# Kernel tuning notes

Hardware: AMD Instinct MI355X
Metric: run time of the kernel (lower is better)

The kernel has to match this reference:

```python
import jax, jax.numpy as jnp
import numpy as np

B, T, H = 2, 2048, 1024
DFF = 4 * H        # dense_mlp hidden width
E = 8              # num_experts_temp
TOP_K = 2


def setup_inputs() -> dict:
    key = jax.random.key(0)
    ks = jax.random.split(key, 6)
    s_h = 1.0 / np.sqrt(H)
    s_f = 1.0 / np.sqrt(DFF)
    return {
        "hidden_states": jax.random.normal(ks[0], (B, T, H), dtype=jnp.float32),
        "router_w": jax.random.normal(ks[1], (E, H), dtype=jnp.float32) * s_h,
        "w1": jax.random.normal(ks[2], (E, H, DFF), dtype=jnp.float32) * s_h,
        "b1": jnp.zeros((E, DFF), dtype=jnp.float32),
        "w2": jax.random.normal(ks[3], (E, DFF, H), dtype=jnp.float32) * s_f,
        "b2": jnp.zeros((E, H), dtype=jnp.float32),
    }


def reference(hidden_states, router_w, w1, b1, w2, b2):
    # Router: [B,T,E]
    router_logits = jnp.einsum("bth,eh->bte", hidden_states, router_w)
    topk_vals, topk_idx = jax.lax.top_k(router_logits, TOP_K)        # [B,T,K]
    topk_w = jax.nn.softmax(topk_vals.astype(jnp.float32), axis=-1)
    topk_w = topk_w.astype(hidden_states.dtype)

    # Dense compute of ALL experts (faithful to the original module).
    h = jnp.einsum("bth,ehf->btef", hidden_states, w1) + b1          # [B,T,E,DFF]
    h = jax.nn.gelu(h)
    expert_out = jnp.einsum("btef,efh->bteh", h, w2) + b2            # [B,T,E,H]

    # Gather top-k experts per token and mix.
    topk_out = jnp.take_along_axis(expert_out, topk_idx[..., None], axis=2)  # [B,T,K,H]
    mixed = jnp.sum(topk_out * topk_w[..., None], axis=2)            # [B,T,H]
    return mixed
```

## Files before the change

kernel.cpp:

```cpp
#include <hip/hip_runtime.h>
#include <hip/hip_bf16.h>
#include <stdint.h>

#define AS1 __attribute__((address_space(1)))
#define AS3 __attribute__((address_space(3)))

typedef __bf16 bf16x8 __attribute__((ext_vector_type(8)));
typedef float floatx4 __attribute__((ext_vector_type(4)));

static constexpr int NTOK = 4096;
static constexpr int H    = 1024;
static constexpr int DFF  = 4096;
static constexpr int E    = 8;
static constexpr int BN   = 128;
static constexpr int RBMAX = 72;

static constexpr size_t OFF_WS     = 0;
static constexpr size_t OFF_XCS    = 67108864;
static constexpr size_t OFF_HS     = 85983232;
static constexpr size_t OFF_P1     = 161480704;
static constexpr size_t OFF_RTIDX  = 180355072;
static constexpr size_t OFF_RTW    = 180387840;
static constexpr size_t OFF_PTOK   = 180420608;
static constexpr size_t OFF_PW     = 180457472;
static constexpr size_t OFF_TOKPOS = 180494336;
static constexpr size_t OFF_CNT    = 180527104;
static constexpr size_t WS_NEED    = 180527232;

__device__ __forceinline__ unsigned short f2bf(float f) {
    __bf16 b = (__bf16)f;
    return __builtin_bit_cast(unsigned short, b);
}
__device__ __forceinline__ float bf2f(unsigned short u) {
    unsigned int v = ((unsigned int)u) << 16;
    return __builtin_bit_cast(float, v);
}

__device__ __forceinline__ void gload16(const void* g, void* l) {
    __builtin_amdgcn_global_load_lds((AS1 void*)g, (AS3 void*)l, 16, 0, 0);
}

__global__ __launch_bounds__(256) void k_router(const float* __restrict__ x,
                                                const float* __restrict__ rw,
                                                int* __restrict__ rt_idx,
                                                float* __restrict__ rt_w,
                                                int* __restrict__ counts) {
    const int wv = threadIdx.x >> 6, ln = threadIdx.x & 63;
    const int t = blockIdx.x * 4 + wv;
    const float* xr = x + (size_t)t * H + ln * 4;
    float4 xv[4];
#pragma unroll
    for (int c = 0; c < 4; ++c) xv[c] = *(const float4*)(xr + c * 256);
    float lg[E];
#pragma unroll
    for (int e = 0; e < E; ++e) {
        const float* rr = rw + (size_t)e * H + ln * 4;
        float acc = 0.f;
#pragma unroll
        for (int c = 0; c < 4; ++c) {
            float4 rv = *(const float4*)(rr + c * 256);
            acc += xv[c].x * rv.x + xv[c].y * rv.y + xv[c].z * rv.z + xv[c].w * rv.w;
        }
#pragma unroll
        for (int s = 32; s > 0; s >>= 1) acc += __shfl_xor(acc, s, 64);
        lg[e] = acc;
    }
    if (ln == 0) {
        int i0 = 0; float v0 = lg[0];
#pragma unroll
        for (int e = 1; e < E; ++e) if (lg[e] > v0) { v0 = lg[e]; i0 = e; }
        int i1 = -1; float v1 = -INFINITY;
#pragma unroll
        for (int e = 0; e < E; ++e) if (e != i0 && lg[e] > v1) { v1 = lg[e]; i1 = e; }
        float e1 = expf(v1 - v0);
        float inv = 1.f / (1.f + e1);
        rt_idx[2 * t] = i0; rt_idx[2 * t + 1] = i1;
        rt_w[2 * t] = inv;  rt_w[2 * t + 1] = e1 * inv;
        atomicAdd(&counts[i0], 1);
        atomicAdd(&counts[i1], 1);
    }
}

__global__ void k_offsets(const int* __restrict__ counts, int* __restrict__ offs) {
    if (threadIdx.x == 0) {
        int o = 0;
        for (int e = 0; e < E; ++e) { offs[e] = o; o += (counts[e] + 127) & ~127; }
        offs[E] = o;
    }
}

__global__ __launch_bounds__(256) void k_scatter(const int* __restrict__ rt_idx,
                                                 const float* __restrict__ rt_w,
                                                 const int* __restrict__ offs,
                                                 int* __restrict__ cursors,
                                                 int* __restrict__ pair_tok,
                                                 float* __restrict__ pair_w,
                                                 int* __restrict__ tok_pos) {
    int t = blockIdx.x * 256 + threadIdx.x;
    if (t >= NTOK) return;
    for (int k = 0; k < 2; ++k) {
        int e = rt_idx[2 * t + k];
        int p = atomicAdd(&cursors[e], 1);
        int pos = offs[e] + p;
        pair_tok[pos] = t;
        pair_w[pos] = rt_w[2 * t + k];
        tok_pos[2 * t + k] = pos;
    }
}

__global__ __launch_bounds__(256) void k_gather(const float* __restrict__ x,
                                                const int* __restrict__ offs,
                                                const int* __restrict__ counts,
                                                const int* __restrict__ pair_tok,
                                                unsigned short* __restrict__ xcs) {
    int pos = blockIdx.x;
    if (pos >= offs[E]) return;
    int e = 0;
    while (e < E - 1 && pos >= offs[e + 1]) ++e;
    bool valid = (pos - offs[e]) < counts[e];
    int tok = valid ? pair_tok[pos] : 0;
    int k0 = threadIdx.x * 4;
    float4 xv = valid ? *(const float4*)(x + (size_t)tok * H + k0)
                      : make_float4(0.f, 0.f, 0.f, 0.f);
    ushort4 o;
    o.x = f2bf(xv.x); o.y = f2bf(xv.y); o.z = f2bf(xv.z); o.w = f2bf(xv.w);
    int rb = pos >> 7, m = pos & 127;
    size_t idx = (((size_t)(rb * 32 + (k0 >> 5)) * 128 + m) * 32) + (((k0 >> 3) & 3) << 3) + (k0 & 7);
    *(ushort4*)(xcs + idx) = o;
}

template <int K, int N>
__global__ __launch_bounds__(256) void k_convert(const float* __restrict__ w,
                                                 unsigned short* __restrict__ ws) {
    constexpr int KB = K / 32, NC = N / 128;
    const int bid = blockIdx.x;
    const int nc = bid % NC, kb = (bid / NC) % KB, e = bid / (NC * KB);
    const int n0 = nc * 128;
    __shared__ float lp[32][128];
    const int tid = threadIdx.x;
    {
        const int kr = tid >> 5;
        const int c4 = (tid & 31) * 4;
        const float* src = w + (size_t)(e * K + kb * 32 + kr) * N + n0 + c4;
#pragma unroll
        for (int c = 0; c < 4; ++c)
            *(float4*)&lp[kr + 8 * c][c4] = *(const float4*)(src + (size_t)(8 * c) * N);
    }
    __syncthreads();
    const size_t base = ((size_t)(e * KB + kb) * N + n0) * 4;
#pragma unroll
    for (int it = 0; it < 2; ++it) {
        const int item = it * 256 + tid;
        const int nl = item >> 2, kq = item & 3;
        union { unsigned short us[8]; uint4 v; } u;
#pragma unroll
        for (int j = 0; j < 8; ++j) u.us[j] = f2bf(lp[kq * 8 + j][nl]);
        *(uint4*)(ws + (base + (size_t)nl * 4 + kq) * 8) = u.v;
    }
}

__global__ __launch_bounds__(256) void k_gemm1(const unsigned short* __restrict__ Xc,
                                               const unsigned short* __restrict__ W1s,
                                               const int* __restrict__ offs,
                                               const float* __restrict__ b1,
                                               unsigned short* __restrict__ Hs) {
    constexpr int KB = H / 32;
    constexpr int MP = 36;
    constexpr int NB = DFF / BN;
    constexpr int CPX = NB * (RBMAX - 1) / 8;
    const int bid = blockIdx.x;
    const int t = (bid & 7) * CPX + (bid >> 3);
    const int rb = t / NB;
    if (rb * 128 >= offs[E]) return;
    int e = 0;
    while (e < E - 1 && rb * 128 >= offs[e + 1]) ++e;
    const int n0 = (t % NB) * BN;

    __shared__ unsigned short smem[4 * 128 * MP];
    unsigned short* lds_a = smem;
    unsigned short* lds_b = smem + 4096;

    const int tid = threadIdx.x;
    const int wv = tid >> 6, ln = tid & 63;
    const int quad = ln >> 4, lr = ln & 15;
    const int wm = (wv & 1) * 64, wn = (wv >> 1) * 64;

    floatx4 acc[4][4];
#pragma unroll
    for (int i = 0; i < 4; ++i)
#pragma unroll
        for (int j = 0; j < 4; ++j) acc[i][j] = (floatx4){0.f, 0.f, 0.f, 0.f};

    const unsigned short* Atile = Xc + (size_t)rb * KB * 4096;
    const unsigned short* Btile = W1s + ((size_t)e * KB * DFF + n0) * 32;

    for (int kb = 0; kb < KB; ++kb) {
        __syncthreads();
        const unsigned short* a_src = Atile + (size_t)kb * 4096 + (wv * 2) * 512 + ln * 8;
        const unsigned short* b_src = Btile + (size_t)kb * DFF * 32 + (wv * 2) * 512 + ln * 8;
#pragma unroll
        for (int c = 0; c < 2; ++c) {
            gload16(a_src + c * 512, &lds_a[(wv * 2 + c) * 512]);
            gload16(b_src + c * 512, &lds_b[(wv * 2 + c) * 512]);
        }
        __syncthreads();
        bf16x8 af[4], bg[4];
#pragma unroll
        for (int i = 0; i < 4; ++i) {
            af[i] = *(const bf16x8*)(lds_a + (wm + i * 16 + lr) * 32 + quad * 8);
            bg[i] = *(const bf16x8*)(lds_b + (wn + i * 16 + lr) * 32 + quad * 8);
        }
#pragma unroll
        for (int i = 0; i < 4; ++i)
#pragma unroll
            for (int j = 0; j < 4; ++j)
                acc[i][j] = __builtin_amdgcn_mfma_f32_16x16x32_bf16(af[i], bg[j], acc[i][j], 0, 0, 0);
    }

    float bj[4];
#pragma unroll
    for (int j = 0; j < 4; ++j) bj[j] = b1[(size_t)e * DFF + n0 + wn + j * 16 + lr];
    __syncthreads();
#pragma unroll
    for (int j = 0; j < 4; ++j) {
        const int fl = wn + j * 16 + lr;
        const int fb = fl >> 5, f5 = fl & 31;
        unsigned short* dst = smem + fb * (128 * MP) + f5;
#pragma unroll
        for (int i = 0; i < 4; ++i) {
#pragma unroll
            for (int r = 0; r < 4; ++r) {
                const int m = wm + i * 16 + quad * 4 + r;
                float v = acc[i][j][r] + bj[j];
                float u = 0.79788456080286535588f * (v + 0.044715f * v * v * v);
                float ez = __expf(2.f * u);
                float g = v * (1.f - 1.f / (ez + 1.f));
                dst[m * MP] = f2bf(g);
            }
        }
    }
    __syncthreads();
    const size_t hsbase = ((size_t)rb * 128 + (n0 >> 5)) * 4096;
#pragma unroll
    for (int it = 0; it < 8; ++it) {
        const int g = (it * 256 + tid) * 8;
        const int fb = g >> 12, rem = g & 4095, m = rem >> 5, f5 = rem & 31;
        const unsigned short* s = smem + fb * (128 * MP) + m * MP + f5;
        uint2 lo = *(const uint2*)s;
        uint2 hi = *(const uint2*)(s + 4);
        *(uint4*)(Hs + hsbase + (size_t)g) = make_uint4(lo.x, lo.y, hi.x, hi.y);
    }
}

__global__ __launch_bounds__(256) void k_gemm2(const unsigned short* __restrict__ Hs,
                                               const unsigned short* __restrict__ W2s,
                                               const int* __restrict__ offs,
                                               const float* __restrict__ b2,
                                               unsigned short* __restrict__ P0,
                                               unsigned short* __restrict__ P1) {
    constexpr int KB = DFF / 32;
    constexpr int KBS = KB / 2;
    constexpr int NB = H / BN;
    constexpr int CPX = NB * (RBMAX - 1) * 2 / 8;
    const int bid = blockIdx.x;
    const int t = (bid & 7) * CPX + (bid >> 3);
    const int yz = t >> 3;
    const int rb = yz % (RBMAX - 1);
    const int ks = yz / (RBMAX - 1);
    if (rb * 128 >= offs[E]) return;
    int e = 0;
    while (e < E - 1 && rb * 128 >= offs[e + 1]) ++e;
    const int n0 = (t & 7) * BN;

    __shared__ unsigned short smem[8192];
    unsigned short* lds_a = smem;
    unsigned short* lds_b = smem + 4096;

    const int tid = threadIdx.x;
    const int wv = tid >> 6, ln = tid & 63;
    const int quad = ln >> 4, lr = ln & 15;
    const int wm = (wv & 1) * 64, wn = (wv >> 1) * 64;

    floatx4 acc[4][4];
#pragma unroll
    for (int i = 0; i < 4; ++i)
#pragma unroll
        for (int j = 0; j < 4; ++j) acc[i][j] = (floatx4){0.f, 0.f, 0.f, 0.f};

    const unsigned short* Atile = Hs + (size_t)rb * KB * 4096;
    const unsigned short* Btile = W2s + ((size_t)e * KB * H + n0) * 32;

    for (int kb = ks * KBS; kb < ks * KBS + KBS; ++kb) {
        __syncthreads();
        const unsigned short* a_src = Atile + (size_t)kb * 4096 + (wv * 2) * 512 + ln * 8;
        const unsigned short* b_src = Btile + (size_t)kb * H * 32 + (wv * 2) * 512 + ln * 8;
#pragma unroll
        for (int c = 0; c < 2; ++c) {
            gload16(a_src + c * 512, &lds_a[(wv * 2 + c) * 512]);
            gload16(b_src + c * 512, &lds_b[(wv * 2 + c) * 512]);
        }
        __syncthreads();
        bf16x8 af[4], bg[4];
#pragma unroll
        for (int i = 0; i < 4; ++i) {
            af[i] = *(const bf16x8*)(lds_a + (wm + i * 16 + lr) * 32 + quad * 8);
            bg[i] = *(const bf16x8*)(lds_b + (wn + i * 16 + lr) * 32 + quad * 8);
        }
#pragma unroll
        for (int i = 0; i < 4; ++i)
#pragma unroll
            for (int j = 0; j < 4; ++j)
                acc[i][j] = __builtin_amdgcn_mfma_f32_16x16x32_bf16(af[i], bg[j], acc[i][j], 0, 0, 0);
    }

    float bj[4];
#pragma unroll
    for (int j = 0; j < 4; ++j)
        bj[j] = (ks == 0) ? b2[(size_t)e * H + n0 + wn + j * 16 + lr] : 0.f;
    unsigned short* P = ks ? P1 : P0;
#pragma unroll
    for (int i = 0; i < 4; ++i) {
#pragma unroll
        for (int r = 0; r < 4; ++r) {
            const int m = wm + i * 16 + quad * 4 + r;
            unsigned short* row = P + (size_t)(rb * 128 + m) * H + n0;
#pragma unroll
            for (int j = 0; j < 4; ++j)
                row[wn + j * 16 + lr] = f2bf(acc[i][j][r] + bj[j]);
        }
    }
}

__global__ __launch_bounds__(256) void k_mix(const unsigned short* __restrict__ P0,
                                             const unsigned short* __restrict__ P1,
                                             const int* __restrict__ tok_pos,
                                             const float* __restrict__ rt_w,
                                             float* __restrict__ out) {
    const int t = blockIdx.x;
    const int c = threadIdx.x * 4;
    const int p0 = tok_pos[2 * t], p1 = tok_pos[2 * t + 1];
    const float w0 = rt_w[2 * t], w1 = rt_w[2 * t + 1];
    ushort4 a0 = *(const ushort4*)(P0 + (size_t)p0 * H + c);
    ushort4 a1 = *(const ushort4*)(P1 + (size_t)p0 * H + c);
    ushort4 b0 = *(const ushort4*)(P0 + (size_t)p1 * H + c);
    ushort4 b1 = *(const ushort4*)(P1 + (size_t)p1 * H + c);
    float4 o;
    o.x = w0 * (bf2f(a0.x) + bf2f(a1.x)) + w1 * (bf2f(b0.x) + bf2f(b1.x));
    o.y = w0 * (bf2f(a0.y) + bf2f(a1.y)) + w1 * (bf2f(b0.y) + bf2f(b1.y));
    o.z = w0 * (bf2f(a0.z) + bf2f(a1.z)) + w1 * (bf2f(b0.z) + bf2f(b1.z));
    o.w = w0 * (bf2f(a0.w) + bf2f(a1.w)) + w1 * (bf2f(b0.w) + bf2f(b1.w));
    *(float4*)(out + (size_t)t * H + c) = o;
}

extern "C" void kernel_launch(void* const* d_in, const int* in_sizes, int n_in,
                              void* d_out, int out_size, void* d_ws, size_t ws_size,
                              hipStream_t stream) {
    const float* x  = (const float*)d_in[0];
    const float* rw = (const float*)d_in[1];
    const float* w1 = (const float*)d_in[2];
    const float* b1 = (const float*)d_in[3];
    const float* w2 = (const float*)d_in[4];
    const float* b2 = (const float*)d_in[5];
    float* out = (float*)d_out;
    char* ws = (char*)d_ws;
    if (ws_size < WS_NEED) return;

    unsigned short* Ws   = (unsigned short*)(ws + OFF_WS);
    unsigned short* XcS  = (unsigned short*)(ws + OFF_XCS);
    unsigned short* Hs   = (unsigned short*)(ws + OFF_HS);
    unsigned short* P1   = (unsigned short*)(ws + OFF_P1);
    int*   rt_idx   = (int*)(ws + OFF_RTIDX);
    float* rt_w     = (float*)(ws + OFF_RTW);
    int*   pair_tok = (int*)(ws + OFF_PTOK);
    float* pair_w   = (float*)(ws + OFF_PW);
    int*   tok_pos  = (int*)(ws + OFF_TOKPOS);
    int*   cnt      = (int*)(ws + OFF_CNT);
    int*   cur      = cnt + 8;
    int*   offs     = cnt + 16;

    hipMemsetAsync(cnt, 0, 128, stream);

    k_router<<<NTOK / 4, 256, 0, stream>>>(x, rw, rt_idx, rt_w, cnt);
    k_offsets<<<1, 64, 0, stream>>>(cnt, offs);
    k_scatter<<<NTOK / 256, 256, 0, stream>>>(rt_idx, rt_w, offs, cur, pair_tok, pair_w, tok_pos);
    k_gather<<<9216, 256, 0, stream>>>(x, offs, cnt, pair_tok, XcS);

    k_convert<H, DFF><<<8 * (H / 32) * (DFF / 128), 256, 0, stream>>>(w1, Ws);
    k_gemm1<<<32 * (RBMAX - 1), 256, 0, stream>>>(XcS, Ws, offs, b1, Hs);

    k_convert<DFF, H><<<8 * (DFF / 32) * (H / 128), 256, 0, stream>>>(w2, Ws);
    k_gemm2<<<8 * (RBMAX - 1) * 2, 256, 0, stream>>>(Hs, Ws, offs, b2, XcS, P1);

    k_mix<<<NTOK, 256, 0, stream>>>(XcS, P1, tok_pos, rt_w, out);
}
```

Measured before the change: 694.7 us.

## Fuse fp32 weight conversion into GEMM loads and split GEMM2 K four ways

Removes the separate weight-conversion kernels. Each GEMM now loads fp32 weights directly into registers, converts them to bf16, and writes them into swizzled LDS, with the next K-block prefetched in registers. GEMM2's K-split grows from 2 to 4 with four partial buffers summed in the mix kernel, and the offsets kernel is replaced by recomputing padded prefixes from the counts. This avoids writing and re-reading the converted weight copy but adds conversion work, strided fp32 loads to the GEMM inner loop, and more partial-sum traffic in the mix.

Result: faster. 665.8 us (-4.2%).

```diff
diff --git a/kernel.cpp b/kernel.cpp
--- a/kernel.cpp
+++ b/kernel.cpp
@@ -13,19 +13,18 @@
 static constexpr int DFF  = 4096;
 static constexpr int E    = 8;
 static constexpr int BN   = 128;
-static constexpr int RBMAX = 72;
-
-static constexpr size_t OFF_WS     = 0;
-static constexpr size_t OFF_XCS    = 67108864;
-static constexpr size_t OFF_HS     = 85983232;
-static constexpr size_t OFF_P1     = 161480704;
-static constexpr size_t OFF_RTIDX  = 180355072;
-static constexpr size_t OFF_RTW    = 180387840;
-static constexpr size_t OFF_PTOK   = 180420608;
-static constexpr size_t OFF_PW     = 180457472;
-static constexpr size_t OFF_TOKPOS = 180494336;
-static constexpr size_t OFF_CNT    = 180527104;
-static constexpr size_t WS_NEED    = 180527232;
+static constexpr int RB   = 71;
+
+static constexpr size_t OFF_XCS    = 0;
+static constexpr size_t OFF_HS     = 18874368;
+static constexpr size_t OFF_P      = 94371840;
+static constexpr size_t PSZ        = 18874368;
+static constexpr size_t OFF_RTIDX  = 169869312;
+static constexpr size_t OFF_RTW    = 169902080;
+static constexpr size_t OFF_PTOK   = 169934848;
+static constexpr size_t OFF_TOKPOS = 169971712;
+static constexpr size_t OFF_CNT    = 170004480;
+static constexpr size_t WS_NEED    = 170004608;
 
 __device__ __forceinline__ unsigned short f2bf(float f) {
     __bf16 b = (__bf16)f;
@@ -38,6 +37,27 @@
 
 __device__ __forceinline__ void gload16(const void* g, void* l) {
     __builtin_amdgcn_global_load_lds((AS1 void*)g, (AS3 void*)l, 16, 0, 0);
+}
+
+__device__ __forceinline__ int find_expert_tot(const int* __restrict__ counts, int row, int* tot_out) {
+    int e = 0, tot = 0;
+#pragma unroll
+    for (int i = 0; i < E; ++i) {
+        int c = (counts[i] + 127) & ~127;
+        if (row >= tot + c) e = i + 1;
+        tot += c;
+    }
+    *tot_out = tot;
+    return e;
+}
+__device__ __forceinline__ int padded_prefix(const int* __restrict__ counts, int e) {
+    int o = 0;
+#pragma unroll
+    for (int i = 0; i < E; ++i) {
+        int c = (counts[i] + 127) & ~127;
+        o += (i < e) ? c : 0;
+    }
+    return o;
 }
 
 __global__ __launch_bounds__(256) void k_router(const float* __restrict__ x,
@@ -81,43 +101,32 @@
     }
 }
 
-__global__ void k_offsets(const int* __restrict__ counts, int* __restrict__ offs) {
-    if (threadIdx.x == 0) {
-        int o = 0;
-        for (int e = 0; e < E; ++e) { offs[e] = o; o += (counts[e] + 127) & ~127; }
-        offs[E] = o;
-    }
-}
-
 __global__ __launch_bounds__(256) void k_scatter(const int* __restrict__ rt_idx,
-                                                 const float* __restrict__ rt_w,
-                                                 const int* __restrict__ offs,
+                                                 const int* __restrict__ counts,
                                                  int* __restrict__ cursors,
                                                  int* __restrict__ pair_tok,
-                                                 float* __restrict__ pair_w,
                                                  int* __restrict__ tok_pos) {
     int t = blockIdx.x * 256 + threadIdx.x;
     if (t >= NTOK) return;
     for (int k = 0; k < 2; ++k) {
         int e = rt_idx[2 * t + k];
         int p = atomicAdd(&cursors[e], 1);
-        int pos = offs[e] + p;
+        int pos = padded_prefix(counts, e) + p;
         pair_tok[pos] = t;
-        pair_w[pos] = rt_w[2 * t + k];
         tok_pos[2 * t + k] = pos;
     }
 }
 
 __global__ __launch_bounds__(256) void k_gather(const float* __restrict__ x,
-                                                const int* __restrict__ offs,
                                                 const int* __restrict__ counts,
                                                 const int* __restrict__ pair_tok,
                                                 unsigned short* __restrict__ xcs) {
     int pos = blockIdx.x;
-    if (pos >= offs[E]) return;
-    int e = 0;
-    while (e < E - 1 && pos >= offs[e + 1]) ++e;
-    bool valid = (pos - offs[e]) < counts[e];
+    int tot;
+    int e = find_expert_tot(counts, pos, &tot);
+    if (pos >= tot) return;
+    int off_e = padded_prefix(counts, e);
+    bool valid = (pos - off_e) < counts[e];
     int tok = valid ? pair_tok[pos] : 0;
     int k0 = threadIdx.x * 4;
     float4 xv = valid ? *(const float4*)(x + (size_t)tok * H + k0)
@@ -125,55 +134,26 @@
     ushort4 o;
     o.x = f2bf(xv.x); o.y = f2bf(xv.y); o.z = f2bf(xv.z); o.w = f2bf(xv.w);
     int rb = pos >> 7, m = pos & 127;
-    size_t idx = (((size_t)(rb * 32 + (k0 >> 5)) * 128 + m) * 32) + (((k0 >> 3) & 3) << 3) + (k0 & 7);
+    size_t idx = (((size_t)(rb * 32 + (k0 >> 5)) * 128 + m) * 32) + (k0 & 31);
     *(ushort4*)(xcs + idx) = o;
 }
 
-template <int K, int N>
-__global__ __launch_bounds__(256) void k_convert(const float* __restrict__ w,
-                                                 unsigned short* __restrict__ ws) {
-    constexpr int KB = K / 32, NC = N / 128;
-    const int bid = blockIdx.x;
-    const int nc = bid % NC, kb = (bid / NC) % KB, e = bid / (NC * KB);
-    const int n0 = nc * 128;
-    __shared__ float lp[32][128];
-    const int tid = threadIdx.x;
-    {
-        const int kr = tid >> 5;
-        const int c4 = (tid & 31) * 4;
-        const float* src = w + (size_t)(e * K + kb * 32 + kr) * N + n0 + c4;
-#pragma unroll
-        for (int c = 0; c < 4; ++c)
-            *(float4*)&lp[kr + 8 * c][c4] = *(const float4*)(src + (size_t)(8 * c) * N);
-    }
-    __syncthreads();
-    const size_t base = ((size_t)(e * KB + kb) * N + n0) * 4;
-#pragma unroll
-    for (int it = 0; it < 2; ++it) {
-        const int item = it * 256 + tid;
-        const int nl = item >> 2, kq = item & 3;
-        union { unsigned short us[8]; uint4 v; } u;
-#pragma unroll
-        for (int j = 0; j < 8; ++j) u.us[j] = f2bf(lp[kq * 8 + j][nl]);
-        *(uint4*)(ws + (base + (size_t)nl * 4 + kq) * 8) = u.v;
-    }
-}
-
 __global__ __launch_bounds__(256) void k_gemm1(const unsigned short* __restrict__ Xc,
-                                               const unsigned short* __restrict__ W1s,
-                                               const int* __restrict__ offs,
+                                               const float* __restrict__ w1,
+                                               const int* __restrict__ counts,
                                                const float* __restrict__ b1,
                                                unsigned short* __restrict__ Hs) {
     constexpr int KB = H / 32;
     constexpr int MP = 36;
     constexpr int NB = DFF / BN;
-    constexpr int CPX = NB * (RBMAX - 1) / 8;
+    constexpr int CPX = NB * RB / 8;
     const int bid = blockIdx.x;
     const int t = (bid & 7) * CPX + (bid >> 3);
     const int rb = t / NB;
-    if (rb * 128 >= offs[E]) return;
-    int e = 0;
-    while (e < E - 1 && rb * 128 >= offs[e + 1]) ++e;
+    const int row = rb * 128;
+    int tot;
+    const int e = find_expert_tot(counts, row, &tot);
+    if (row >= tot) return;
     const int n0 = (t % NB) * BN;
 
     __shared__ unsigned short smem[4 * 128 * MP];
@@ -184,6 +164,12 @@
     const int wv = tid >> 6, ln = tid & 63;
     const int quad = ln >> 4, lr = ln & 15;
     const int wm = (wv & 1) * 64, wn = (wv >> 1) * 64;
+    const int bswz = quad ^ ((lr >> 1) & 3);
+
+    const int skq = wv, sn = ln;
+    const int sswz = skq ^ ((sn >> 1) & 3);
+    const int wb1 = sn * 32 + sswz * 8;
+    const int wb2 = wb1 + 2048;
 
     floatx4 acc[4][4];
 #pragma unroll
@@ -192,23 +178,42 @@
         for (int j = 0; j < 4; ++j) acc[i][j] = (floatx4){0.f, 0.f, 0.f, 0.f};
 
     const unsigned short* Atile = Xc + (size_t)rb * KB * 4096;
-    const unsigned short* Btile = W1s + ((size_t)e * KB * DFF + n0) * 32;
+    const float* Bsrc = w1 + ((size_t)e * H + skq * 8) * DFF + n0 + sn;
+
+    float br[16];
+#pragma unroll
+    for (int j = 0; j < 8; ++j) {
+        br[j]     = Bsrc[(size_t)j * DFF];
+        br[8 + j] = Bsrc[(size_t)j * DFF + 64];
+    }
 
     for (int kb = 0; kb < KB; ++kb) {
         __syncthreads();
+        {
+            union { unsigned short us[8]; uint4 v; } u1, u2;
+#pragma unroll
+            for (int j = 0; j < 8; ++j) { u1.us[j] = f2bf(br[j]); u2.us[j] = f2bf(br[8 + j]); }
+            *(uint4*)(lds_b + wb1) = u1.v;
+            *(uint4*)(lds_b + wb2) = u2.v;
+        }
         const unsigned short* a_src = Atile + (size_t)kb * 4096 + (wv * 2) * 512 + ln * 8;
-        const unsigned short* b_src = Btile + (size_t)kb * DFF * 32 + (wv * 2) * 512 + ln * 8;
-#pragma unroll
-        for (int c = 0; c < 2; ++c) {
-            gload16(a_src + c * 512, &lds_a[(wv * 2 + c) * 512]);
-            gload16(b_src + c * 512, &lds_b[(wv * 2 + c) * 512]);
+        gload16(a_src, &lds_a[(wv * 2) * 512]);
+        gload16(a_src + 512, &lds_a[(wv * 2 + 1) * 512]);
+        {
+            const int kbn = (kb + 1 < KB) ? kb + 1 : kb;
+            const float* bs = Bsrc + (size_t)kbn * 32 * DFF;
+#pragma unroll
+            for (int j = 0; j < 8; ++j) {
+                br[j]     = bs[(size_t)j * DFF];
+                br[8 + j] = bs[(size_t)j * DFF + 64];
+            }
         }
         __syncthreads();
         bf16x8 af[4], bg[4];
 #pragma unroll
         for (int i = 0; i < 4; ++i) {
             af[i] = *(const bf16x8*)(lds_a + (wm + i * 16 + lr) * 32 + quad * 8);
-            bg[i] = *(const bf16x8*)(lds_b + (wn + i * 16 + lr) * 32 + quad * 8);
+            bg[i] = *(const bf16x8*)(lds_b + (wn + i * 16 + lr) * 32 + bswz * 8);
         }
 #pragma unroll
         for (int i = 0; i < 4; ++i)
@@ -253,24 +258,26 @@
 }
 
 __global__ __launch_bounds__(256) void k_gemm2(const unsigned short* __restrict__ Hs,
-                                               const unsigned short* __restrict__ W2s,
-                                               const int* __restrict__ offs,
+                                               const float* __restrict__ w2,
+                                               const int* __restrict__ counts,
                                                const float* __restrict__ b2,
-                                               unsigned short* __restrict__ P0,
-                                               unsigned short* __restrict__ P1) {
+                                               unsigned short* __restrict__ Pb) {
     constexpr int KB = DFF / 32;
-    constexpr int KBS = KB / 2;
+    constexpr int NSPLIT = 4;
+    constexpr int KBS = KB / NSPLIT;
     constexpr int NB = H / BN;
-    constexpr int CPX = NB * (RBMAX - 1) * 2 / 8;
+    constexpr int CPX = NB * RB * NSPLIT / 8;
     const int bid = blockIdx.x;
     const int t = (bid & 7) * CPX + (bid >> 3);
-    const int yz = t >> 3;
-    const int rb = yz % (RBMAX - 1);
-    const int ks = yz / (RBMAX - 1);
-    if (rb * 128 >= offs[E]) return;
-    int e = 0;
-    while (e < E - 1 && rb * 128 >= offs[e + 1]) ++e;
-    const int n0 = (t & 7) * BN;
+    const int nb = t & 7;
+    const int rest = t >> 3;
+    const int rb = rest % RB;
+    const int ks = rest / RB;
+    const int row = rb * 128;
+    int tot;
+    const int e = find_expert_tot(counts, row, &tot);
+    if (row >= tot) return;
+    const int n0 = nb * BN;
 
     __shared__ unsigned short smem[8192];
     unsigned short* lds_a = smem;
@@ -280,6 +287,12 @@
     const int wv = tid >> 6, ln = tid & 63;
     const int quad = ln >> 4, lr = ln & 15;
     const int wm = (wv & 1) * 64, wn = (wv >> 1) * 64;
+    const int bswz = quad ^ ((lr >> 1) & 3);
+
+    const int skq = wv, sn = ln;
+    const int sswz = skq ^ ((sn >> 1) & 3);
+    const int wb1 = sn * 32 + sswz * 8;
+    const int wb2 = wb1 + 2048;
 
     floatx4 acc[4][4];
 #pragma unroll
@@ -287,24 +300,43 @@
 #pragma unroll
         for (int j = 0; j < 4; ++j) acc[i][j] = (floatx4){0.f, 0.f, 0.f, 0.f};
 
-    const unsigned short* Atile = Hs + (size_t)rb * KB * 4096;
-    const unsigned short* Btile = W2s + ((size_t)e * KB * H + n0) * 32;
-
-    for (int kb = ks * KBS; kb < ks * KBS + KBS; ++kb) {
+    const unsigned short* Atile = Hs + ((size_t)rb * KB + ks * KBS) * 4096;
+    const float* Bsrc = w2 + ((size_t)e * DFF + ks * KBS * 32 + skq * 8) * H + n0 + sn;
+
+    float br[16];
+#pragma unroll
+    for (int j = 0; j < 8; ++j) {
+        br[j]     = Bsrc[(size_t)j * H];
+        br[8 + j] = Bsrc[(size_t)j * H + 64];
+    }
+
+    for (int kb = 0; kb < KBS; ++kb) {
         __syncthreads();
+        {
+            union { unsigned short us[8]; uint4 v; } u1, u2;
+#pragma unroll
+            for (int j = 0; j < 8; ++j) { u1.us[j] = f2bf(br[j]); u2.us[j] = f2bf(br[8 + j]); }
+            *(uint4*)(lds_b + wb1) = u1.v;
+            *(uint4*)(lds_b + wb2) = u2.v;
+        }
         const unsigned short* a_src = Atile + (size_t)kb * 4096 + (wv * 2) * 512 + ln * 8;
-        const unsigned short* b_src = Btile + (size_t)kb * H * 32 + (wv * 2) * 512 + ln * 8;
-#pragma unroll
-        for (int c = 0; c < 2; ++c) {
-            gload16(a_src + c * 512, &lds_a[(wv * 2 + c) * 512]);
-            gload16(b_src + c * 512, &lds_b[(wv * 2 + c) * 512]);
+        gload16(a_src, &lds_a[(wv * 2) * 512]);
+        gload16(a_src + 512, &lds_a[(wv * 2 + 1) * 512]);
+        {
+            const int kbn = (kb + 1 < KBS) ? kb + 1 : kb;
+            const float* bs = Bsrc + (size_t)kbn * 32 * H;
+#pragma unroll
+            for (int j = 0; j < 8; ++j) {
+                br[j]     = bs[(size_t)j * H];
+                br[8 + j] = bs[(size_t)j * H + 64];
+            }
         }
         __syncthreads();
         bf16x8 af[4], bg[4];
 #pragma unroll
         for (int i = 0; i < 4; ++i) {
             af[i] = *(const bf16x8*)(lds_a + (wm + i * 16 + lr) * 32 + quad * 8);
-            bg[i] = *(const bf16x8*)(lds_b + (wn + i * 16 + lr) * 32 + quad * 8);
+            bg[i] = *(const bf16x8*)(lds_b + (wn + i * 16 + lr) * 32 + bswz * 8);
         }
 #pragma unroll
         for (int i = 0; i < 4; ++i)
@@ -317,22 +349,21 @@
 #pragma unroll
     for (int j = 0; j < 4; ++j)
         bj[j] = (ks == 0) ? b2[(size_t)e * H + n0 + wn + j * 16 + lr] : 0.f;
-    unsigned short* P = ks ? P1 : P0;
+    unsigned short* P = Pb + (size_t)ks * (PSZ / 2);
 #pragma unroll
     for (int i = 0; i < 4; ++i) {
 #pragma unroll
         for (int r = 0; r < 4; ++r) {
             const int m = wm + i * 16 + quad * 4 + r;
-            unsigned short* row = P + (size_t)(rb * 128 + m) * H + n0;
+            unsigned short* rowp = P + (size_t)(rb * 128 + m) * H + n0;
 #pragma unroll
             for (int j = 0; j < 4; ++j)
-                row[wn + j * 16 + lr] = f2bf(acc[i][j][r] + bj[j]);
-        }
-    }
-}
-
-__global__ __launch_bounds__(256) void k_mix(const unsigned short* __restrict__ P0,
-                                             const unsigned short* __restrict__ P1,
+                rowp[wn + j * 16 + lr] = f2bf(acc[i][j][r] + bj[j]);
+        }
+    }
+}
+
+__global__ __launch_bounds__(256) void k_mix(const unsigned short* __restrict__ Pb,
                                              const int* __restrict__ tok_pos,
                                              const float* __restrict__ rt_w,
                                              float* __restrict__ out) {
@@ -340,15 +371,21 @@
     const int c = threadIdx.x * 4;
     const int p0 = tok_pos[2 * t], p1 = tok_pos[2 * t + 1];
     const float w0 = rt_w[2 * t], w1 = rt_w[2 * t + 1];
-    ushort4 a0 = *(const ushort4*)(P0 + (size_t)p0 * H + c);
-    ushort4 a1 = *(const ushort4*)(P1 + (size_t)p0 * H + c);
-    ushort4 b0 = *(const ushort4*)(P0 + (size_t)p1 * H + c);
-    ushort4 b1 = *(const ushort4*)(P1 + (size_t)p1 * H + c);
+    float4 s0 = make_float4(0.f, 0.f, 0.f, 0.f);
+    float4 s1 = make_float4(0.f, 0.f, 0.f, 0.f);
+#pragma unroll
+    for (int q = 0; q < 4; ++q) {
+        const unsigned short* P = Pb + (size_t)q * (PSZ / 2);
+        ushort4 a = *(const ushort4*)(P + (size_t)p0 * H + c);
+        ushort4 b = *(const ushort4*)(P + (size_t)p1 * H + c);
+        s0.x += bf2f(a.x); s0.y += bf2f(a.y); s0.z += bf2f(a.z); s0.w += bf2f(a.w);
+        s1.x += bf2f(b.x); s1.y += bf2f(b.y); s1.z += bf2f(b.z); s1.w += bf2f(b.w);
+    }
     float4 o;
-    o.x = w0 * (bf2f(a0.x) + bf2f(a1.x)) + w1 * (bf2f(b0.x) + bf2f(b1.x));
-    o.y = w0 * (bf2f(a0.y) + bf2f(a1.y)) + w1 * (bf2f(b0.y) + bf2f(b1.y));
-    o.z = w0 * (bf2f(a0.z) + bf2f(a1.z)) + w1 * (bf2f(b0.z) + bf2f(b1.z));
-    o.w = w0 * (bf2f(a0.w) + bf2f(a1.w)) + w1 * (bf2f(b0.w) + bf2f(b1.w));
+    o.x = w0 * s0.x + w1 * s1.x;
+    o.y = w0 * s0.y + w1 * s1.y;
+    o.z = w0 * s0.z + w1 * s1.z;
+    o.w = w0 * s0.w + w1 * s1.w;
     *(float4*)(out + (size_t)t * H + c) = o;
 }
 
@@ -365,31 +402,24 @@
     char* ws = (char*)d_ws;
     if (ws_size < WS_NEED) return;
 
-    unsigned short* Ws   = (unsigned short*)(ws + OFF_WS);
-    unsigned short* XcS  = (unsigned short*)(ws + OFF_XCS);
-    unsigned short* Hs   = (unsigned short*)(ws + OFF_HS);
-    unsigned short* P1   = (unsigned short*)(ws + OFF_P1);
+    unsigned short* XcS = (unsigned short*)(ws + OFF_XCS);
+    unsigned short* Hs  = (unsigned short*)(ws + OFF_HS);
+    unsigned short* Pb  = (unsigned short*)(ws + OFF_P);
     int*   rt_idx   = (int*)(ws + OFF_RTIDX);
     float* rt_w     = (float*)(ws + OFF_RTW);
     int*   pair_tok = (int*)(ws + OFF_PTOK);
-    float* pair_w   = (float*)(ws + OFF_PW);
     int*   tok_pos  = (int*)(ws + OFF_TOKPOS);
     int*   cnt      = (int*)(ws + OFF_CNT);
     int*   cur      = cnt + 8;
-    int*   offs     = cnt + 16;
 
     hipMemsetAsync(cnt, 0, 128, stream);
 
     k_router<<<NTOK / 4, 256, 0, stream>>>(x, rw, rt_idx, rt_w, cnt);
-    k_offsets<<<1, 64, 0, stream>>>(cnt, offs);
-    k_scatter<<<NTOK / 256, 256, 0, stream>>>(rt_idx, rt_w, offs, cur, pair_tok, pair_w, tok_pos);
-    k_gather<<<9216, 256, 0, stream>>>(x, offs, cnt, pair_tok, XcS);
-
-    k_convert<H, DFF><<<8 * (H / 32) * (DFF / 128), 256, 0, stream>>>(w1, Ws);
-    k_gemm1<<<32 * (RBMAX - 1), 256, 0, stream>>>(XcS, Ws, offs, b1, Hs);
-
-    k_convert<DFF, H><<<8 * (DFF / 32) * (H / 128), 256, 0, stream>>>(w2, Ws);
-    k_gemm2<<<8 * (RBMAX - 1) * 2, 256, 0, stream>>>(Hs, Ws, offs, b2, XcS, P1);
-
-    k_mix<<<NTOK, 256, 0, stream>>>(XcS, P1, tok_pos, rt_w, out);
-}
+    k_scatter<<<NTOK / 256, 256, 0, stream>>>(rt_idx, cnt, cur, pair_tok, tok_pos);
+    k_gather<<<RB * 128, 256, 0, stream>>>(x, cnt, pair_tok, XcS);
+
+    k_gemm1<<<(DFF / BN) * RB, 256, 0, stream>>>(XcS, w1, cnt, b1, Hs);
+    k_gemm2<<<(H / BN) * RB * 4, 256, 0, stream>>>(Hs, w2, cnt, b2, Pb);
+
+    k_mix<<<NTOK, 256, 0, stream>>>(Pb, tok_pos, rt_w, out);
+}
```
